# Performance work log

Measured on AMD Instinct MI355X. Metric: run time of the kernel, lower is better.

## Reference

```python
import jax, jax.numpy as jnp
import numpy as np

B, T, C, H, O = 256, 256, 32, 512, 32
OUT_TIME = 32


def setup_inputs() -> dict:
    key = jax.random.key(0)
    ks = jax.random.split(key, 10)
    times = jnp.arange(T, dtype=jnp.float32)
    coeffs = jax.random.normal(ks[0], (B, T, C), jnp.float32)
    final_index = jax.random.randint(ks[1], (B,), 0, T)
    dW = jax.random.normal(ks[2], (T - 1, B, H), jnp.float32)  # unit-normal; scaled by sqrt(dt) inside
    s = lambda k, shape, fan: jax.random.normal(k, shape, jnp.float32) / np.float32(np.sqrt(fan))
    return {
        "times": times, "coeffs": coeffs, "final_index": final_index, "dW": dW,
        "W_init": s(ks[3], (C, H), C), "b_init": jnp.zeros((H,), jnp.float32),
        "W1": s(ks[4], (H + C, H), H + C), "b1": jnp.zeros((H,), jnp.float32),
        "W2": s(ks[5], (H, H), H), "b2": jnp.zeros((H,), jnp.float32),
        "Wg": s(ks[6], (H, H), H), "bg": jnp.zeros((H,), jnp.float32),
        "Wh1": s(ks[7], (H, H), H), "bh1": jnp.zeros((H,), jnp.float32),
        "Wh2": s(ks[8], (H, O), H), "bh2": jnp.zeros((O,), jnp.float32),
    }


def reference(times, coeffs, final_index, dW, W_init, b_init, W1, b1, W2, b2, Wg, bg, Wh1, bh1, Wh2, bh2):
    # dt = max(min(diff(times)), 0.001)  (Euler method default in the torch module)
    dt = jnp.maximum(jnp.min(times[1:] - times[:-1]), jnp.float32(0.001))
    sqdt = jnp.sqrt(dt)

    x_seq = jnp.transpose(coeffs, (1, 0, 2))  # [T, B, C] control path at grid points
    # z0 = initial_network(X.evaluate(times[0]))
    z0 = x_seq[0] @ W_init + b_init  # [B, H]

    def step(y, inp):
        xk, dWk = inp  # [B, C], [B, H]
        h = jnp.tanh(jnp.concatenate([y, xk], axis=-1) @ W1 + b1)
        f = jnp.tanh(h @ W2 + b2)                # drift
        g = jax.nn.sigmoid(y @ Wg + bg)          # diagonal diffusion
        y_next = y + f * dt + g * (sqdt * dWk)   # Euler-Maruyama step
        return y_next, y_next

    _, zs = jax.lax.scan(step, z0, (x_seq[:-1], dW))  # zs: [T-1, B, H]
    z = jnp.concatenate([z0[None], zs], axis=0)       # [T, B, H]
    z = jnp.transpose(z, (1, 0, 2))                   # [B, T, H]  (transpose loop in torch code)
    z_tail = z[:, z.shape[1] - OUT_TIME:, :]          # last output_time steps
    return jax.nn.relu(z_tail @ Wh1 + bh1) @ Wh2 + bh2  # [B, OUT_TIME, O]
```

## Files before the change

kernel.cpp:

```cpp
#include <hip/hip_runtime.h>
#include <stdint.h>
#include <stddef.h>

typedef __attribute__((ext_vector_type(8))) short short8;
typedef __attribute__((ext_vector_type(2))) short short2v;
typedef __attribute__((ext_vector_type(8))) _Float16 half8;
typedef __attribute__((ext_vector_type(4))) float f32x4;
typedef unsigned long long ull;

#define T_  256
#define B_  256
#define C_  32
#define H_  512
#define O_  32
#define KB1 17
#define NT1 64
#define KB2 16
#define NT2 32

__device__ __forceinline__ short f2h(float f) {
  _Float16 h = (_Float16)f;
  return __builtin_bit_cast(short, h);
}
__device__ __forceinline__ void f2hl(float f, short& hi, short& lo) {
  _Float16 h = (_Float16)f;
  _Float16 l = (_Float16)(f - (float)h);
  hi = __builtin_bit_cast(short, h);
  lo = __builtin_bit_cast(short, l);
}
__device__ __forceinline__ unsigned int pack_hl(float f) {
  short h, l;
  f2hl(f, h, l);
  return (unsigned int)(unsigned short)h | ((unsigned int)(unsigned short)l << 16);
}
__device__ __forceinline__ float fast_tanh(float x) {
  float e = __expf(2.0f * x);
  return 1.0f - 2.0f / (e + 1.0f);
}
__device__ __forceinline__ float fast_sigmoid(float x) {
  return 1.0f / (1.0f + __expf(-x));
}
__device__ __forceinline__ f32x4 mfma16(half8 a, half8 b, f32x4 c) {
  return __builtin_amdgcn_mfma_f32_16x16x32_f16(a, b, c, 0, 0, 0);
}
__device__ __forceinline__ half8 ld8(const short* p) { return *(const half8*)p; }

__device__ __forceinline__ void st_coh(unsigned int* p, unsigned int v) {
  __hip_atomic_store(p, v, __ATOMIC_RELAXED, __HIP_MEMORY_SCOPE_AGENT);
}
__device__ __forceinline__ ull ld_coh(const ull* p) {
  return __hip_atomic_load(p, __ATOMIC_RELAXED, __HIP_MEMORY_SCOPE_AGENT);
}

__device__ __forceinline__ void stage_pk(const ull* src, short* hi, short* lo,
                                         int stride, int tid) {
  ull v[16];
  #pragma unroll
  for (int i = 0; i < 16; ++i) v[i] = ld_coh(src + i * 256 + tid);
  #pragma unroll
  for (int i = 0; i < 16; ++i) {
    int chunk = i * 256 + tid;
    int row = chunk >> 8, col = (chunk & 255) << 1;
    unsigned int u0 = (unsigned int)v[i], u1 = (unsigned int)(v[i] >> 32);
    short2v h2, l2;
    h2[0] = (short)(u0 & 0xffffu); h2[1] = (short)(u1 & 0xffffu);
    l2[0] = (short)(u0 >> 16);     l2[1] = (short)(u1 >> 16);
    *(short2v*)(hi + row * stride + col) = h2;
    *(short2v*)(lo + row * stride + col) = l2;
  }
}

__device__ __forceinline__ void bg_barrier(unsigned int* cnt, unsigned int target) {
  __syncthreads();
  if (threadIdx.x == 0) {
    __hip_atomic_fetch_add(cnt, 1u, __ATOMIC_RELAXED, __HIP_MEMORY_SCOPE_AGENT);
    while (__hip_atomic_load(cnt, __ATOMIC_RELAXED, __HIP_MEMORY_SCOPE_AGENT) < target)
      __builtin_amdgcn_s_sleep(1);
  }
  __syncthreads();
}

__global__ void pack_b1s(const float* __restrict__ W1, const float* __restrict__ Wg,
                         short* __restrict__ hi, short* __restrict__ lo) {
  int gid = blockIdx.x * 256 + threadIdx.x;
  if (gid >= KB1 * NT1 * 512) return;
  int j = gid & 7, lane = (gid >> 3) & 63, tile = gid >> 9;
  int nt = tile % NT1, kb = tile / NT1;
  int k = kb * 32 + ((lane >> 4) << 3) + j;
  int n = ((nt & 31) << 4) + (lane & 15);
  float v = 0.f;
  if (nt < 32)      v = W1[k * H_ + n];
  else if (k < H_)  v = Wg[k * H_ + n];
  short h, l;
  f2hl(v, h, l);
  hi[gid] = h; lo[gid] = l;
}

__global__ void pack_s(const float* __restrict__ src, short* __restrict__ hi,
                       short* __restrict__ lo, int Ksrc, int Nsrc, int KB, int NT) {
  int gid = blockIdx.x * 256 + threadIdx.x;
  if (gid >= KB * NT * 512) return;
  int j = gid & 7, lane = (gid >> 3) & 63, tile = gid >> 9;
  int nt = tile % NT, kb = tile / NT;
  int k = kb * 32 + ((lane >> 4) << 3) + j;
  int n = (nt << 4) + (lane & 15);
  float v = (k < Ksrc && n < Nsrc) ? src[k * Nsrc + n] : 0.f;
  short h, l;
  f2hl(v, h, l);
  hi[gid] = h;
  if (lo) lo[gid] = l;
}

__global__ __launch_bounds__(256, 1) void sde_kernel(
    const float* __restrict__ times, const float* __restrict__ coeffs,
    const float* __restrict__ dW,
    const float* __restrict__ b_init, const float* __restrict__ b1,
    const float* __restrict__ b2, const float* __restrict__ bgb,
    const short* __restrict__ B1h, const short* __restrict__ B1l,
    const short* __restrict__ W2h, const short* __restrict__ W2l,
    const short* __restrict__ WIh, const short* __restrict__ WIl,
    unsigned int* __restrict__ y_pk, unsigned int* __restrict__ h_pk,
    short* __restrict__ zt, unsigned int* __restrict__ cnt_base) {
  __shared__ short yx_hi[16][552];
  __shared__ short yx_lo[16][552];
  __shared__ short hh_hi[16][520];
  __shared__ short hh_lo[16][520];
  __shared__ float g_x[16][32];
  __shared__ float redbuf[4];

  const int tid = threadIdx.x;
  const int w = tid >> 6, l = tid & 63;
  const int ra = l & 15, kq = l >> 4;
  const int bid = blockIdx.x;
  const int bg = bid & 15, cg = bid >> 4;
  const int R0 = bg << 4;
  unsigned int* cnt = cnt_base + bg * 32;

  const int nt1w = (w < 2) ? (2 * cg + w) : (32 + 2 * cg + (w - 2));
  const int extcol = nt1w * 16 + ra;
  const int ntF = 2 * cg + (w & 1);
  const int fcol = ntF * 16 + ra;

  float d = 1e30f;
  if (tid < T_ - 1) d = times[tid + 1] - times[tid];
  #pragma unroll
  for (int s = 32; s >= 1; s >>= 1) d = fminf(d, __shfl_xor(d, s, 64));
  if (l == 0) redbuf[w] = d;

  half8 wb1h[17], wb1l[17];
  #pragma unroll
  for (int kb = 0; kb < 17; ++kb) {
    const size_t off = ((size_t)(kb * 64 + nt1w) << 9) + (l << 3);
    wb1h[kb] = ld8(B1h + off);
    wb1l[kb] = ld8(B1l + off);
  }
  half8 ww2h[16], ww2l[16];
  if (w < 2) {
    #pragma unroll
    for (int kb = 0; kb < 16; ++kb) {
      const size_t off = ((size_t)(kb * 32 + ntF) << 9) + (l << 3);
      ww2h[kb] = ld8(W2h + off);
      ww2l[kb] = ld8(W2l + off);
    }
  }

  if (tid < 64) {
    int row = tid >> 2, cc = (tid & 3) << 3;
    const float* xb = coeffs + (size_t)(R0 + row) * (T_ * C_) + cc;
    #pragma unroll
    for (int j = 0; j < 8; ++j) {
      short h, lo;
      f2hl(xb[j], h, lo);
      yx_hi[row][512 + cc + j] = h;
      yx_lo[row][512 + cc + j] = lo;
    }
  }
  __syncthreads();
  float m = fminf(fminf(redbuf[0], redbuf[1]), fminf(redbuf[2], redbuf[3]));
  const float dt = fmaxf(m, 0.001f);
  const float sq = sqrtf(dt);

  const float b1v = (w < 2) ? b1[extcol] : 0.f;
  const float bgv = (w >= 2) ? bgb[extcol - 512] : 0.f;
  const float b2v = (w < 2) ? b2[fcol] : 0.f;

  float yr[4] = {0.f, 0.f, 0.f, 0.f};
  if (w < 2) {
    half8 ah = ld8(&yx_hi[ra][512 + (kq << 3)]);
    half8 al = ld8(&yx_lo[ra][512 + (kq << 3)]);
    half8 bh = ld8(WIh + ((size_t)ntF << 9) + (l << 3));
    half8 bl = ld8(WIl + ((size_t)ntF << 9) + (l << 3));
    f32x4 Z = {0.f, 0.f, 0.f, 0.f};
    Z = mfma16(ah, bh, Z); Z = mfma16(al, bh, Z); Z = mfma16(ah, bl, Z);
    float bi = b_init[fcol];
    #pragma unroll
    for (int r = 0; r < 4; ++r) {
      yr[r] = Z[r] + bi;
      st_coh(&y_pk[(size_t)(R0 + (kq << 2) + r) * H_ + fcol], pack_hl(yr[r]));
    }
  }
  bg_barrier(cnt, 16u);

  for (int k = 0; k < T_ - 1; ++k) {
    float dwv[4];
    if (w < 2) {
      const float* dwb = dW + ((size_t)k * B_ + R0) * H_ + fcol;
      #pragma unroll
      for (int r = 0; r < 4; ++r)
        dwv[r] = __builtin_nontemporal_load(dwb + ((kq << 2) + r) * H_);
    }
    stage_pk((const ull*)y_pk + R0 * 256, &yx_hi[0][0], &yx_lo[0][0], 552, tid);
    if (tid < 64) {
      int row = tid >> 2, cc = (tid & 3) << 3;
      const float* xb = coeffs + (size_t)(R0 + row) * (T_ * C_) + (size_t)k * C_ + cc;
      #pragma unroll
      for (int j = 0; j < 8; ++j) {
        short h, lo;
        f2hl(xb[j], h, lo);
        yx_hi[row][512 + cc + j] = h;
        yx_lo[row][512 + cc + j] = lo;
      }
    }
    __syncthreads();
    f32x4 A = {0.f, 0.f, 0.f, 0.f};
    #pragma unroll
    for (int kb = 0; kb < 17; ++kb) {
      half8 ah = ld8(&yx_hi[ra][(kb << 5) + (kq << 3)]);
      half8 al = ld8(&yx_lo[ra][(kb << 5) + (kq << 3)]);
      A = mfma16(ah, wb1h[kb], A);
      A = mfma16(al, wb1h[kb], A);
      A = mfma16(ah, wb1l[kb], A);
    }
    if (w < 2) {
      #pragma unroll
      for (int r = 0; r < 4; ++r) {
        float h = fast_tanh(A[r] + b1v);
        st_coh(&h_pk[(size_t)(R0 + (kq << 2) + r) * H_ + extcol], pack_hl(h));
      }
    } else {
      #pragma unroll
      for (int r = 0; r < 4; ++r)
        g_x[(kq << 2) + r][((w - 2) << 4) + ra] = fast_sigmoid(A[r] + bgv);
    }
    bg_barrier(cnt, 16u * (2u * (unsigned)k + 2u));
    stage_pk((const ull*)h_pk + R0 * 256, &hh_hi[0][0], &hh_lo[0][0], 520, tid);
    __syncthreads();
    if (w < 2) {
      f32x4 F = {0.f, 0.f, 0.f, 0.f};
      #pragma unroll
      for (int kb = 0; kb < 16; ++kb) {
        half8 ah = ld8(&hh_hi[ra][(kb << 5) + (kq << 3)]);
        half8 al = ld8(&hh_lo[ra][(kb << 5) + (kq << 3)]);
        F = mfma16(ah, ww2h[kb], F);
        F = mfma16(al, ww2h[kb], F);
        F = mfma16(ah, ww2l[kb], F);
      }
      #pragma unroll
      for (int r = 0; r < 4; ++r) {
        float f = fast_tanh(F[r] + b2v);
        float g = g_x[(kq << 2) + r][((w & 1) << 4) + ra];
        yr[r] += f * dt + g * (sq * dwv[r]);
        st_coh(&y_pk[(size_t)(R0 + (kq << 2) + r) * H_ + fcol], pack_hl(yr[r]));
      }
      if (k >= T_ - 1 - O_) {
        int t = k - (T_ - 1 - O_);
        #pragma unroll
        for (int r = 0; r < 4; ++r)
          zt[((size_t)(R0 + (kq << 2) + r) * O_ + t) * H_ + fcol] = f2h(yr[r]);
      }
    }
    bg_barrier(cnt, 16u * (2u * (unsigned)k + 3u));
  }
}

__global__ __launch_bounds__(256) void head_kernel(
    const short* __restrict__ zt, const short* __restrict__ Wh1p,
    const short* __restrict__ Wh2p, const float* __restrict__ bh1,
    const float* __restrict__ bh2, float* __restrict__ out) {
  __shared__ short a_lds[32][520];
  __shared__ short h2_lds[32][520];
  const int tid = threadIdx.x;
  const int w = tid >> 6, l = tid & 63;
  const int ra = l & 15, kq = l >> 4;
  const int r0 = blockIdx.x << 5;

  const short* zb = zt + (size_t)r0 * H_;
  #pragma unroll
  for (int i = 0; i < 8; ++i) {
    int cidx = i * 256 + tid;
    int row = cidx >> 6, cc = (cidx & 63) << 3;
    *(short8*)&a_lds[row][cc] = *(const short8*)(zb + row * H_ + cc);
  }
  __syncthreads();

  f32x4 acc[2][8];
  #pragma unroll
  for (int mt = 0; mt < 2; ++mt)
    #pragma unroll
    for (int i = 0; i < 8; ++i) acc[mt][i] = (f32x4){0.f, 0.f, 0.f, 0.f};
  for (int kb = 0; kb < 16; ++kb) {
    half8 a0 = ld8(&a_lds[ra][(kb << 5) + (kq << 3)]);
    half8 a1 = ld8(&a_lds[16 + ra][(kb << 5) + (kq << 3)]);
    const short* bp = Wh1p + (size_t)kb * (32 * 512) + (l << 3);
    #pragma unroll
    for (int i = 0; i < 8; ++i) {
      half8 b = ld8(bp + ((8 * w + i) << 9));
      acc[0][i] = mfma16(a0, b, acc[0][i]);
      acc[1][i] = mfma16(a1, b, acc[1][i]);
    }
  }
  #pragma unroll
  for (int i = 0; i < 8; ++i) {
    int col = ((8 * w + i) << 4) + ra;
    float bb = bh1[col];
    #pragma unroll
    for (int mt = 0; mt < 2; ++mt)
      #pragma unroll
      for (int r = 0; r < 4; ++r) {
        float h = acc[mt][i][r] + bb;
        h = h > 0.f ? h : 0.f;
        h2_lds[(mt << 4) + (kq << 2) + r][col] = f2h(h);
      }
  }
  __syncthreads();

  {
    int mt = w >> 1, nt = w & 1;
    f32x4 F = {0.f, 0.f, 0.f, 0.f};
    for (int kb = 0; kb < 16; ++kb) {
      half8 a = ld8(&h2_lds[(mt << 4) + ra][(kb << 5) + (kq << 3)]);
      half8 b = ld8(Wh2p + (size_t)((kb * 2 + nt) * 64 + l) * 8);
      F = mfma16(a, b, F);
    }
    int col = (nt << 4) + ra;
    float bb = bh2[col];
    #pragma unroll
    for (int r = 0; r < 4; ++r)
      out[(size_t)(r0 + (mt << 4) + (kq << 2) + r) * O_ + col] = F[r] + bb;
  }
}

extern "C" void kernel_launch(void* const* d_in, const int* in_sizes, int n_in,
                              void* d_out, int out_size, void* d_ws, size_t ws_size,
                              hipStream_t stream) {
  (void)in_sizes; (void)n_in; (void)out_size; (void)ws_size;
  const float* times  = (const float*)d_in[0];
  const float* coeffs = (const float*)d_in[1];
  const float* dW     = (const float*)d_in[3];
  const float* W_init = (const float*)d_in[4];
  const float* b_init = (const float*)d_in[5];
  const float* W1     = (const float*)d_in[6];
  const float* b1     = (const float*)d_in[7];
  const float* W2     = (const float*)d_in[8];
  const float* b2     = (const float*)d_in[9];
  const float* Wg     = (const float*)d_in[10];
  const float* bg     = (const float*)d_in[11];
  const float* Wh1    = (const float*)d_in[12];
  const float* bh1    = (const float*)d_in[13];
  const float* Wh2    = (const float*)d_in[14];
  const float* bh2    = (const float*)d_in[15];
  float* out = (float*)d_out;
  char* ws = (char*)d_ws;

  short* B1h  = (short*)(ws + 0);
  short* B1l  = (short*)(ws + 1114112);
  short* W2h  = (short*)(ws + 2228224);
  short* W2l  = (short*)(ws + 2752512);
  short* WIh  = (short*)(ws + 3276800);
  short* WIl  = (short*)(ws + 3309568);
  short* Wh1p = (short*)(ws + 3342336);
  short* Wh2p = (short*)(ws + 3866624);
  unsigned int* y_pk = (unsigned int*)(ws + 3899392);
  unsigned int* h_pk = (unsigned int*)(ws + 4423680);
  short* zt   = (short*)(ws + 4947968);
  unsigned int* cnt = (unsigned int*)(ws + 13336576);

  pack_b1s<<<2176, 256, 0, stream>>>(W1, Wg, B1h, B1l);
  pack_s  <<<1024, 256, 0, stream>>>(W2, W2h, W2l, 512, 512, 16, 32);
  pack_s  <<<64,   256, 0, stream>>>(W_init, WIh, WIl, 32, 512, 1, 32);
  pack_s  <<<1024, 256, 0, stream>>>(Wh1, Wh1p, (short*)nullptr, 512, 512, 16, 32);
  pack_s  <<<64,   256, 0, stream>>>(Wh2, Wh2p, (short*)nullptr, 512, 32, 16, 2);

  hipMemsetAsync(ws + 13336576, 0, 2048, stream);

  sde_kernel<<<256, 256, 0, stream>>>(times, coeffs, dW, b_init, b1, b2, bg,
                                      B1h, B1l, W2h, W2l, WIh, WIl,
                                      y_pk, h_pk, zt, cnt);
  head_kernel<<<256, 256, 0, stream>>>(zt, Wh1p, Wh2p, bh1, bh2, out);
}
```

Before: 1.502 ms.

## Widen LDS staging stores, split MFMA accumulators, prefetch next-step control input

The staging routine now loads two adjacent packed words per thread and writes 64-bit hi/lo LDS stores instead of 32-bit ones. The MFMA chains for the W1/Wg and W2 products are split into three independent accumulators, which breaks the serial dependency between the hi/lo partial products. Loading and splitting the next step's coeffs row is moved out of the critical staging path into idle wave 2 during the drift phase. The cost is more accumulator registers and a slightly different order of floating-point summation.

```diff
diff --git a/kernel.cpp b/kernel.cpp
--- a/kernel.cpp
+++ b/kernel.cpp
@@ -3,7 +3,6 @@
 #include <stddef.h>
 
 typedef __attribute__((ext_vector_type(8))) short short8;
-typedef __attribute__((ext_vector_type(2))) short short2v;
 typedef __attribute__((ext_vector_type(8))) _Float16 half8;
 typedef __attribute__((ext_vector_type(4))) float f32x4;
 typedef unsigned long long ull;
@@ -52,21 +51,27 @@
   return __hip_atomic_load(p, __ATOMIC_RELAXED, __HIP_MEMORY_SCOPE_AGENT);
 }
 
-__device__ __forceinline__ void stage_pk(const ull* src, short* hi, short* lo,
+__device__ __forceinline__ void stage_pl(const ull* src, short* hi, short* lo,
                                          int stride, int tid) {
   ull v[16];
   #pragma unroll
-  for (int i = 0; i < 16; ++i) v[i] = ld_coh(src + i * 256 + tid);
-  #pragma unroll
-  for (int i = 0; i < 16; ++i) {
-    int chunk = i * 256 + tid;
-    int row = chunk >> 8, col = (chunk & 255) << 1;
-    unsigned int u0 = (unsigned int)v[i], u1 = (unsigned int)(v[i] >> 32);
-    short2v h2, l2;
-    h2[0] = (short)(u0 & 0xffffu); h2[1] = (short)(u1 & 0xffffu);
-    l2[0] = (short)(u0 >> 16);     l2[1] = (short)(u1 >> 16);
-    *(short2v*)(hi + row * stride + col) = h2;
-    *(short2v*)(lo + row * stride + col) = l2;
+  for (int i = 0; i < 8; ++i) {
+    int p = i * 256 + tid;
+    v[2 * i]     = ld_coh(src + 2 * p);
+    v[2 * i + 1] = ld_coh(src + 2 * p + 1);
+  }
+  #pragma unroll
+  for (int i = 0; i < 8; ++i) {
+    int p = i * 256 + tid;
+    int row = p >> 7, col4 = (p & 127) << 2;
+    unsigned int u0 = (unsigned int)v[2 * i],     u1 = (unsigned int)(v[2 * i] >> 32);
+    unsigned int u2 = (unsigned int)v[2 * i + 1], u3 = (unsigned int)(v[2 * i + 1] >> 32);
+    unsigned int hiA = (u0 & 0xffffu) | (u1 << 16);
+    unsigned int hiB = (u2 & 0xffffu) | (u3 << 16);
+    unsigned int loA = (u0 >> 16) | (u1 & 0xffff0000u);
+    unsigned int loB = (u2 >> 16) | (u3 & 0xffff0000u);
+    *(ull*)(hi + row * stride + col4) = (ull)hiA | ((ull)hiB << 32);
+    *(ull*)(lo + row * stride + col4) = (ull)loA | ((ull)loB << 32);
   }
 }
 
@@ -167,13 +172,15 @@
   if (tid < 64) {
     int row = tid >> 2, cc = (tid & 3) << 3;
     const float* xb = coeffs + (size_t)(R0 + row) * (T_ * C_) + cc;
+    short8 hi, lo;
     #pragma unroll
     for (int j = 0; j < 8; ++j) {
-      short h, lo;
-      f2hl(xb[j], h, lo);
-      yx_hi[row][512 + cc + j] = h;
-      yx_lo[row][512 + cc + j] = lo;
-    }
+      short h, l2;
+      f2hl(xb[j], h, l2);
+      hi[j] = h; lo[j] = l2;
+    }
+    *(short8*)&yx_hi[row][512 + cc] = hi;
+    *(short8*)&yx_lo[row][512 + cc] = lo;
   }
   __syncthreads();
   float m = fminf(fminf(redbuf[0], redbuf[1]), fminf(redbuf[2], redbuf[3]));
@@ -209,55 +216,45 @@
       for (int r = 0; r < 4; ++r)
         dwv[r] = __builtin_nontemporal_load(dwb + ((kq << 2) + r) * H_);
     }
-    stage_pk((const ull*)y_pk + R0 * 256, &yx_hi[0][0], &yx_lo[0][0], 552, tid);
-    if (tid < 64) {
-      int row = tid >> 2, cc = (tid & 3) << 3;
-      const float* xb = coeffs + (size_t)(R0 + row) * (T_ * C_) + (size_t)k * C_ + cc;
-      #pragma unroll
-      for (int j = 0; j < 8; ++j) {
-        short h, lo;
-        f2hl(xb[j], h, lo);
-        yx_hi[row][512 + cc + j] = h;
-        yx_lo[row][512 + cc + j] = lo;
-      }
-    }
+    stage_pl((const ull*)y_pk + R0 * 256, &yx_hi[0][0], &yx_lo[0][0], 552, tid);
     __syncthreads();
-    f32x4 A = {0.f, 0.f, 0.f, 0.f};
+    f32x4 Aa = {0.f, 0.f, 0.f, 0.f}, Ab = Aa, Ac = Aa;
     #pragma unroll
     for (int kb = 0; kb < 17; ++kb) {
       half8 ah = ld8(&yx_hi[ra][(kb << 5) + (kq << 3)]);
       half8 al = ld8(&yx_lo[ra][(kb << 5) + (kq << 3)]);
-      A = mfma16(ah, wb1h[kb], A);
-      A = mfma16(al, wb1h[kb], A);
-      A = mfma16(ah, wb1l[kb], A);
+      Aa = mfma16(ah, wb1h[kb], Aa);
+      Ab = mfma16(al, wb1h[kb], Ab);
+      Ac = mfma16(ah, wb1l[kb], Ac);
     }
     if (w < 2) {
       #pragma unroll
       for (int r = 0; r < 4; ++r) {
-        float h = fast_tanh(A[r] + b1v);
+        float h = fast_tanh((Aa[r] + Ab[r]) + Ac[r] + b1v);
         st_coh(&h_pk[(size_t)(R0 + (kq << 2) + r) * H_ + extcol], pack_hl(h));
       }
     } else {
       #pragma unroll
       for (int r = 0; r < 4; ++r)
-        g_x[(kq << 2) + r][((w - 2) << 4) + ra] = fast_sigmoid(A[r] + bgv);
+        g_x[(kq << 2) + r][((w - 2) << 4) + ra] =
+            fast_sigmoid((Aa[r] + Ab[r]) + Ac[r] + bgv);
     }
     bg_barrier(cnt, 16u * (2u * (unsigned)k + 2u));
-    stage_pk((const ull*)h_pk + R0 * 256, &hh_hi[0][0], &hh_lo[0][0], 520, tid);
+    stage_pl((const ull*)h_pk + R0 * 256, &hh_hi[0][0], &hh_lo[0][0], 520, tid);
     __syncthreads();
     if (w < 2) {
-      f32x4 F = {0.f, 0.f, 0.f, 0.f};
+      f32x4 Fa = {0.f, 0.f, 0.f, 0.f}, Fb = Fa, Fc = Fa;
       #pragma unroll
       for (int kb = 0; kb < 16; ++kb) {
         half8 ah = ld8(&hh_hi[ra][(kb << 5) + (kq << 3)]);
         half8 al = ld8(&hh_lo[ra][(kb << 5) + (kq << 3)]);
-        F = mfma16(ah, ww2h[kb], F);
-        F = mfma16(al, ww2h[kb], F);
-        F = mfma16(ah, ww2l[kb], F);
+        Fa = mfma16(ah, ww2h[kb], Fa);
+        Fb = mfma16(al, ww2h[kb], Fb);
+        Fc = mfma16(ah, ww2l[kb], Fc);
       }
       #pragma unroll
       for (int r = 0; r < 4; ++r) {
-        float f = fast_tanh(F[r] + b2v);
+        float f = fast_tanh((Fa[r] + Fb[r]) + Fc[r] + b2v);
         float g = g_x[(kq << 2) + r][((w & 1) << 4) + ra];
         yr[r] += f * dt + g * (sq * dwv[r]);
         st_coh(&y_pk[(size_t)(R0 + (kq << 2) + r) * H_ + fcol], pack_hl(yr[r]));
@@ -268,6 +265,19 @@
         for (int r = 0; r < 4; ++r)
           zt[((size_t)(R0 + (kq << 2) + r) * O_ + t) * H_ + fcol] = f2h(yr[r]);
       }
+    } else if (w == 2 && k < T_ - 2) {
+      int row = l >> 2, cc = (l & 3) << 3;
+      const float* xb =
+          coeffs + (size_t)(R0 + row) * (T_ * C_) + (size_t)(k + 1) * C_ + cc;
+      short8 hi, lo;
+      #pragma unroll
+      for (int j = 0; j < 8; ++j) {
+        short h, l2;
+        f2hl(xb[j], h, l2);
+        hi[j] = h; lo[j] = l2;
+      }
+      *(short8*)&yx_hi[row][512 + cc] = hi;
+      *(short8*)&yx_lo[row][512 + cc] = lo;
     }
     bg_barrier(cnt, 16u * (2u * (unsigned)k + 3u));
   }
```

New measurement: 1.511 ms (median of 2 runs). No clear change (+0.6%).
